# Performance work log

Measured on AMD Instinct MI355X. Metric: run time of the kernel, lower is better.

## Reference

```python
import jax, jax.numpy as jnp
import numpy as np

# dims
B, QL, KL = 2, 1024, 4096
HID = 2048            # hidden_size
H, HD, RD = 16, 128, 64   # heads, head_dim, rope_dim
G = 4                 # gla_num_groups
HPG = H // G          # heads_per_group
QLR = 512             # q low-rank (W_dQ out)
LAT = 256             # latent_dim_per_group
KVP = G * LAT         # kv_proj_dim
EPS = 1e-6


def rmsnorm(x, w):
    var = jnp.mean(jnp.square(x.astype(jnp.float32)), axis=-1, keepdims=True)
    return (x * jax.lax.rsqrt(var + EPS)).astype(x.dtype) * w


def setup_inputs() -> dict:
    key = jax.random.key(0)
    ks = jax.random.split(key, 8)
    s = 0.02
    return {
        "x_q": jax.random.normal(ks[0], (B, QL, HID), jnp.float32),
        "x_kv": jax.random.normal(ks[1], (B, KL, HID), jnp.float32),
        "W_dQ": jax.random.normal(ks[2], (HID, QLR), jnp.float32) * s,
        "q_norm_w": jnp.ones((QLR,), jnp.float32),
        "W_uQ": jax.random.normal(ks[3], (QLR, H * (HD + RD)), jnp.float32) * s,
        "W_dKV": jax.random.normal(ks[4], (HID, KVP + RD), jnp.float32) * s,
        "kv_norm_w": jnp.ones((G, LAT), jnp.float32),
        "W_ukv": jax.random.normal(ks[5], (G, LAT, HPG * 2 * HD), jnp.float32) * s,
        "W_o": jax.random.normal(ks[6], (H * HD, HID), jnp.float32) * s,
    }


def reference(x_q, x_kv, W_dQ, q_norm_w, W_uQ, W_dKV, kv_norm_w, W_ukv, W_o):
    b, ql, _ = x_q.shape
    kl = x_kv.shape[1]
    # --- query path: down-proj -> RMSNorm -> up-proj -> drop rope dims ---
    q = rmsnorm(x_q @ W_dQ, q_norm_w)                       # [b, ql, QLR]
    q = (q @ W_uQ).reshape(b, ql, H, HD + RD)[..., :HD]     # [b, ql, H, HD]
    # --- kv path: down-proj -> slice -> per-group RMSNorm -> grouped up-proj ---
    ckv = (x_kv @ W_dKV)[..., :KVP].reshape(b, kl, G, LAT)  # [b, kl, G, LAT]
    ckv = rmsnorm(ckv, kv_norm_w)                           # weight [G, LAT] broadcasts
    kv = jnp.einsum("bsgl,gld->bsgd", ckv, W_ukv)           # [b, kl, G, HPG*2*HD]
    kv = kv.reshape(b, kl, H, 2 * HD)                       # group-major head order
    k, v = kv[..., :HD], kv[..., HD:]
    # --- SDPA (no mask, non-causal) ---
    scale = 1.0 / np.sqrt(HD).astype(np.float32)
    scores = jnp.einsum("bqhd,bkhd->bhqk", q, k) * scale    # [b, H, ql, kl]
    p = jax.nn.softmax(scores, axis=-1)
    out = jnp.einsum("bhqk,bkhd->bqhd", p, v).reshape(b, ql, H * HD)
    return out @ W_o
```

## Files before the change

### kernel.cpp

```cpp
#include <hip/hip_runtime.h>
#include <hip/hip_bf16.h>
#include <math.h>


typedef __attribute__((ext_vector_type(8))) short short8;
typedef __attribute__((ext_vector_type(4))) float f32x4;

__device__ __forceinline__ ushort f2bf(float x) {
    __hip_bfloat16 h = __float2bfloat16(x);
    return *reinterpret_cast<ushort*>(&h);
}

__global__ __launch_bounds__(256) void cast_bf16(const float* __restrict__ src,
        ushort* __restrict__ dst)
{
    size_t i = ((size_t)blockIdx.x * 256 + threadIdx.x) * 8;
    float4 a = *(const float4*)(src + i);
    float4 b = *(const float4*)(src + i + 4);
    ushort u[8] = {f2bf(a.x), f2bf(a.y), f2bf(a.z), f2bf(a.w),
                   f2bf(b.x), f2bf(b.y), f2bf(b.z), f2bf(b.w)};
    *(uint4*)(dst + i) = *(uint4*)u;
}

__global__ __launch_bounds__(256) void transpose_cast(const float* __restrict__ src,
        ushort* __restrict__ dst, int srl, int dstld, int remap,
        long src_z, long dst_z)
{
    __shared__ ushort tile[64][68];
    const int k0 = blockIdx.x * 64;
    const int n0 = blockIdx.y * 64;
    src += (size_t)blockIdx.z * src_z;
    dst += (size_t)blockIdx.z * dst_z;
    const int cb = n0 + (remap ? (n0 >> 7) * 64 : 0);
    const int t = threadIdx.x;
    {
        int r = t >> 4, c4 = t & 15;
        #pragma unroll
        for (int i = 0; i < 4; ++i) {
            float4 v = *(const float4*)(src + (size_t)(k0 + r + 16 * i) * srl + cb + c4 * 4);
            tile[r + 16 * i][c4 * 4 + 0] = f2bf(v.x);
            tile[r + 16 * i][c4 * 4 + 1] = f2bf(v.y);
            tile[r + 16 * i][c4 * 4 + 2] = f2bf(v.z);
            tile[r + 16 * i][c4 * 4 + 3] = f2bf(v.w);
        }
    }
    __syncthreads();
    {
        int n = t >> 4, k4 = t & 15;
        #pragma unroll
        for (int i = 0; i < 4; ++i) {
            ushort4 v;
            v.x = tile[k4 * 4 + 0][n + 16 * i];
            v.y = tile[k4 * 4 + 1][n + 16 * i];
            v.z = tile[k4 * 4 + 2][n + 16 * i];
            v.w = tile[k4 * 4 + 3][n + 16 * i];
            *(ushort4*)(dst + (size_t)(n0 + n + 16 * i) * dstld + k0 + k4 * 4) = v;
        }
    }
}

__global__ __launch_bounds__(256) void gemm_mfma(const ushort* __restrict__ A,
        const ushort* __restrict__ Bt, void* __restrict__ Cv,
        int M, int N, int K, int lda, int ldb, int ldc, int obf16, float scale)
{
    __shared__ ushort As[128][72];
    __shared__ ushort Bs[128][72];
    const int tid = threadIdx.x;
    const int w = tid >> 6, lane = tid & 63;
    const int quad = lane >> 4, l16 = lane & 15;
    const int wm = (w >> 1) * 64, wn = (w & 1) * 64;
    const int m0 = blockIdx.y * 128, n0 = blockIdx.x * 128;

    f32x4 acc[4][4];
    #pragma unroll
    for (int i = 0; i < 4; ++i)
        #pragma unroll
        for (int j = 0; j < 4; ++j) acc[i][j] = (f32x4){0.f, 0.f, 0.f, 0.f};

    const int str = tid >> 3;
    const int stc = (tid & 7) * 8;

    for (int k0 = 0; k0 < K; k0 += 64) {
        __syncthreads();
        #pragma unroll
        for (int i = 0; i < 4; ++i) {
            int r = str + 32 * i;
            *(uint4*)&As[r][stc] = *(const uint4*)(A + (size_t)(m0 + r) * lda + k0 + stc);
            *(uint4*)&Bs[r][stc] = *(const uint4*)(Bt + (size_t)(n0 + r) * ldb + k0 + stc);
        }
        __syncthreads();
        #pragma unroll
        for (int kc = 0; kc < 2; ++kc) {
            short8 af[4], bf[4];
            #pragma unroll
            for (int i = 0; i < 4; ++i) {
                af[i] = *(const short8*)&As[wm + i * 16 + l16][kc * 32 + quad * 8];
                bf[i] = *(const short8*)&Bs[wn + i * 16 + l16][kc * 32 + quad * 8];
            }
            #pragma unroll
            for (int i = 0; i < 4; ++i)
                #pragma unroll
                for (int j = 0; j < 4; ++j)
                    acc[i][j] = __builtin_amdgcn_mfma_f32_16x16x32_bf16(af[i], bf[j], acc[i][j], 0, 0, 0);
        }
    }
    if (!obf16) {
        float* C = (float*)Cv;
        #pragma unroll
        for (int i = 0; i < 4; ++i)
            #pragma unroll
            for (int r = 0; r < 4; ++r) {
                float* cp = C + (size_t)(m0 + wm + i * 16 + quad * 4 + r) * ldc + n0 + wn + l16;
                #pragma unroll
                for (int j = 0; j < 4; ++j) cp[j * 16] = acc[i][j][r] * scale;
            }
    } else {
        ushort* C = (ushort*)Cv;
        #pragma unroll
        for (int i = 0; i < 4; ++i)
            #pragma unroll
            for (int r = 0; r < 4; ++r) {
                ushort* cp = C + (size_t)(m0 + wm + i * 16 + quad * 4 + r) * ldc + n0 + wn + l16;
                #pragma unroll
                for (int j = 0; j < 4; ++j) cp[j * 16] = f2bf(acc[i][j][r] * scale);
            }
    }
}

__global__ __launch_bounds__(256) void rms_q_wave(const float* __restrict__ x,
        const float* __restrict__ w, ushort* __restrict__ dst)
{
    const int row = blockIdx.x * 4 + (threadIdx.x >> 6);
    const int lane = threadIdx.x & 63;
    const float* p = x + (size_t)row * 512;
    float4 v0 = *(const float4*)(p + lane * 4);
    float4 v1 = *(const float4*)(p + 256 + lane * 4);
    float ss = v0.x*v0.x + v0.y*v0.y + v0.z*v0.z + v0.w*v0.w
             + v1.x*v1.x + v1.y*v1.y + v1.z*v1.z + v1.w*v1.w;
    #pragma unroll
    for (int m = 1; m < 64; m <<= 1) ss += __shfl_xor(ss, m);
    float inv = rsqrtf(ss * (1.f / 512.f) + 1e-6f);
    float4 w0 = *(const float4*)(w + lane * 4);
    float4 w1 = *(const float4*)(w + 256 + lane * 4);
    ushort* dp = dst + (size_t)row * 512;
    ushort4 o0, o1;
    o0.x = f2bf(v0.x * inv * w0.x); o0.y = f2bf(v0.y * inv * w0.y);
    o0.z = f2bf(v0.z * inv * w0.z); o0.w = f2bf(v0.w * inv * w0.w);
    o1.x = f2bf(v1.x * inv * w1.x); o1.y = f2bf(v1.y * inv * w1.y);
    o1.z = f2bf(v1.z * inv * w1.z); o1.w = f2bf(v1.w * inv * w1.w);
    *(ushort4*)(dp + lane * 4)       = o0;
    *(ushort4*)(dp + 256 + lane * 4) = o1;
}

__global__ __launch_bounds__(256) void rms_kv_wave(const float* __restrict__ x,
        const float* __restrict__ w, ushort* __restrict__ dst)
{
    const int idx = blockIdx.x * 4 + (threadIdx.x >> 6);
    const int lane = threadIdx.x & 63;
    const int r = idx >> 2, g = idx & 3;
    const float* p = x + (size_t)r * 1024 + g * 256;
    float4 v = *(const float4*)(p + lane * 4);
    float ss = v.x*v.x + v.y*v.y + v.z*v.z + v.w*v.w;
    #pragma unroll
    for (int m = 1; m < 64; m <<= 1) ss += __shfl_xor(ss, m);
    float inv = rsqrtf(ss * (1.f / 256.f) + 1e-6f);
    float4 wv = *(const float4*)(w + g * 256 + lane * 4);
    ushort4 o;
    o.x = f2bf(v.x * inv * wv.x); o.y = f2bf(v.y * inv * wv.y);
    o.z = f2bf(v.z * inv * wv.z); o.w = f2bf(v.w * inv * wv.w);
    *(ushort4*)(dst + (size_t)r * 1024 + g * 256 + lane * 4) = o;
}

__global__ __launch_bounds__(256) void transpose_v(const ushort* __restrict__ KVb,
                                                   ushort* __restrict__ Vt)
{
    __shared__ ushort tile[64][66];
    const int s0 = blockIdx.x * 64;
    const int d0 = blockIdx.y * 64;
    const int bh = blockIdx.z;
    const int b = bh >> 4, h = bh & 15, g = h >> 2, p = h & 3;
    const int t = threadIdx.x;
    const ushort* src = KVb + (size_t)g * 8388608ull + (size_t)(b * 4096) * 1024 + p * 256 + 128;
    {
        int sl = t >> 4, c4 = t & 15;
        #pragma unroll
        for (int i = 0; i < 4; ++i) {
            int s = sl + 16 * i;
            ushort4 v = *(const ushort4*)(src + (size_t)(s0 + s) * 1024 + d0 + c4 * 4);
            tile[s][c4 * 4 + 0] = v.x; tile[s][c4 * 4 + 1] = v.y;
            tile[s][c4 * 4 + 2] = v.z; tile[s][c4 * 4 + 3] = v.w;
        }
    }
    __syncthreads();
    {
        int dl = t >> 4, s4 = t & 15;
        ushort* dst = Vt + (size_t)(b * 16 + h) * 128 * 4096;
        #pragma unroll
        for (int i = 0; i < 4; ++i) {
            int d = dl + 16 * i;
            ushort4 v;
            v.x = tile[s4 * 4 + 0][d]; v.y = tile[s4 * 4 + 1][d];
            v.z = tile[s4 * 4 + 2][d]; v.w = tile[s4 * 4 + 3][d];
            *(ushort4*)(dst + (size_t)(d0 + d) * 4096 + s0 + s4 * 4) = v;
        }
    }
}

__global__ __launch_bounds__(256) void attn_mfma_split(const ushort* __restrict__ Qb,
        const ushort* __restrict__ KVb, const ushort* __restrict__ Vt,
        float* __restrict__ Opart, float* __restrict__ ml)
{
    __shared__ ushort Ks[64][136];
    __shared__ ushort VsT[128][72];
    __shared__ ushort Ps[4][16][72];

    const int q0 = blockIdx.x * 64;
    const int h = blockIdx.y;
    const int b = blockIdx.z >> 1, chunk = blockIdx.z & 1;
    const int g = h >> 2, p = h & 3;
    const int tid = threadIdx.x;
    const int w = tid >> 6, lane = tid & 63;
    const int quad = lane >> 4, l16 = lane & 15;
    const int sbase = chunk * 2048;

    const ushort* qg = Qb + (size_t)(b * 1024 + q0) * 2048 + h * 128;
    const ushort* kg = KVb + (size_t)g * 8388608ull + (size_t)(b * 4096 + sbase) * 1024 + p * 256;
    const ushort* vg = Vt + (size_t)(b * 16 + h) * 128 * 4096 + sbase;

    {
        int r = tid >> 4, c8 = tid & 15;
        #pragma unroll
        for (int i = 0; i < 4; ++i)
            *(uint4*)&Ks[r + 16 * i][c8 * 8] =
                *(const uint4*)(qg + (size_t)(r + 16 * i) * 2048 + c8 * 8);
    }
    __syncthreads();
    short8 qf[4];
    {
        int qr = w * 16 + l16;
        #pragma unroll
        for (int kc = 0; kc < 4; ++kc)
            qf[kc] = *(const short8*)&Ks[qr][kc * 32 + quad * 8];
    }

    f32x4 accO[8];
    float m_i[4], l_i[4];
    #pragma unroll
    for (int dt = 0; dt < 8; ++dt) accO[dt] = (f32x4){0.f, 0.f, 0.f, 0.f};
    #pragma unroll
    for (int r = 0; r < 4; ++r) { m_i[r] = -INFINITY; l_i[r] = 0.f; }

    for (int s0 = 0; s0 < 2048; s0 += 64) {
        __syncthreads();
        {
            int r = tid >> 4, c8 = tid & 15;
            #pragma unroll
            for (int i = 0; i < 4; ++i)
                *(uint4*)&Ks[r + 16 * i][c8 * 8] =
                    *(const uint4*)(kg + (size_t)(s0 + r + 16 * i) * 1024 + c8 * 8);
            int d = tid >> 3, s8 = tid & 7;
            #pragma unroll
            for (int i = 0; i < 4; ++i)
                *(uint4*)&VsT[d + 32 * i][s8 * 8] =
                    *(const uint4*)(vg + (size_t)(d + 32 * i) * 4096 + s0 + s8 * 8);
        }
        __syncthreads();
        f32x4 accS[4];
        #pragma unroll
        for (int st = 0; st < 4; ++st) accS[st] = (f32x4){0.f, 0.f, 0.f, 0.f};
        #pragma unroll
        for (int kc = 0; kc < 4; ++kc) {
            #pragma unroll
            for (int st = 0; st < 4; ++st) {
                short8 kf = *(const short8*)&Ks[st * 16 + l16][kc * 32 + quad * 8];
                accS[st] = __builtin_amdgcn_mfma_f32_16x16x32_bf16(qf[kc], kf, accS[st], 0, 0, 0);
            }
        }
        #pragma unroll
        for (int r = 0; r < 4; ++r) {
            float tm = fmaxf(fmaxf(accS[0][r], accS[1][r]), fmaxf(accS[2][r], accS[3][r]));
            #pragma unroll
            for (int msk = 1; msk < 16; msk <<= 1) tm = fmaxf(tm, __shfl_xor(tm, msk));
            float mn = fmaxf(m_i[r], tm);
            float alpha = __expf(m_i[r] - mn);
            float rs = 0.f;
            #pragma unroll
            for (int st = 0; st < 4; ++st) {
                float e = __expf(accS[st][r] - mn);
                rs += e;
                Ps[w][quad * 4 + r][st * 16 + l16] = f2bf(e);
            }
            #pragma unroll
            for (int msk = 1; msk < 16; msk <<= 1) rs += __shfl_xor(rs, msk);
            l_i[r] = l_i[r] * alpha + rs;
            m_i[r] = mn;
            #pragma unroll
            for (int dt = 0; dt < 8; ++dt) accO[dt][r] *= alpha;
        }
        __syncthreads();
        short8 pf[2];
        #pragma unroll
        for (int sc = 0; sc < 2; ++sc)
            pf[sc] = *(const short8*)&Ps[w][l16][sc * 32 + quad * 8];
        #pragma unroll
        for (int sc = 0; sc < 2; ++sc) {
            #pragma unroll
            for (int dt = 0; dt < 8; ++dt) {
                short8 vf = *(const short8*)&VsT[dt * 16 + l16][sc * 32 + quad * 8];
                accO[dt] = __builtin_amdgcn_mfma_f32_16x16x32_bf16(pf[sc], vf, accO[dt], 0, 0, 0);
            }
        }
    }
    const int qrow = q0 + w * 16 + quad * 4;
    float* ob = Opart + (size_t)((chunk * 2 + b) * 1024 + qrow) * 2048 + h * 128 + l16;
    #pragma unroll
    for (int r = 0; r < 4; ++r)
        #pragma unroll
        for (int dt = 0; dt < 8; ++dt)
            ob[(size_t)r * 2048 + dt * 16] = accO[dt][r];
    if (l16 == 0) {
        #pragma unroll
        for (int r = 0; r < 4; ++r) {
            size_t mi = ((size_t)((chunk * 2 + b) * 1024 + qrow + r) * 16 + h) * 2;
            ml[mi] = m_i[r];
            ml[mi + 1] = l_i[r];
        }
    }
}

__global__ __launch_bounds__(256) void attn_merge(const float* __restrict__ Opart,
        const float* __restrict__ ml, ushort* __restrict__ Om)
{
    const int idx = blockIdx.x * 4 + (threadIdx.x >> 6);
    const int lane = threadIdx.x & 63;
    const int h = idx & 15;
    const int q = (idx >> 4) & 1023;
    const int b = idx >> 14;

    size_t m1i = ((size_t)((0 * 2 + b) * 1024 + q) * 16 + h) * 2;
    size_t m2i = ((size_t)((1 * 2 + b) * 1024 + q) * 16 + h) * 2;
    float m1 = ml[m1i], l1 = ml[m1i + 1];
    float m2 = ml[m2i], l2 = ml[m2i + 1];
    float M = fmaxf(m1, m2);
    float w1 = __expf(m1 - M), w2 = __expf(m2 - M);
    float invL = 1.f / (l1 * w1 + l2 * w2);

    const float* o1 = Opart + (size_t)((0 * 2 + b) * 1024 + q) * 2048 + h * 128;
    const float* o2 = Opart + (size_t)((1 * 2 + b) * 1024 + q) * 2048 + h * 128;
    ushort* ob = Om + (size_t)(b * 1024 + q) * 2048 + h * 128;
    ob[lane]      = f2bf((o1[lane]      * w1 + o2[lane]      * w2) * invL);
    ob[lane + 64] = f2bf((o1[lane + 64] * w1 + o2[lane + 64] * w2) * invL);
}

extern "C" void kernel_launch(void* const* d_in, const int* in_sizes, int n_in,
                              void* d_out, int out_size, void* d_ws, size_t ws_size,
                              hipStream_t stream)
{
    (void)in_sizes; (void)n_in; (void)out_size; (void)ws_size;
    const float* x_q       = (const float*)d_in[0];
    const float* x_kv      = (const float*)d_in[1];
    const float* W_dQ      = (const float*)d_in[2];
    const float* q_norm_w  = (const float*)d_in[3];
    const float* W_uQ      = (const float*)d_in[4];
    const float* W_dKV     = (const float*)d_in[5];
    const float* kv_norm_w = (const float*)d_in[6];
    const float* W_ukv     = (const float*)d_in[7];
    const float* W_o       = (const float*)d_in[8];
    float* out = (float*)d_out;

    float* ws = (float*)d_ws;
    ushort* xkvb       = (ushort*)ws;
    ushort* attn_out_b = (ushort*)ws;
    float*  mlbuf      = ws + 2097152ull;
    ushort* Wot        = (ushort*)(ws + 4194304ull);
    float*  ckv        = ws + 8388608ull;
    float*  Opart      = ws + 8388608ull;
    ushort* xqb        = (ushort*)(ws + 8388608ull);
    ushort* WdQt       = (ushort*)(ws + 10485760ull);
    float*  q_lat      = ws + 11010048ull;
    ushort* q_lat_b    = (ushort*)(ws + 12058624ull);
    ushort* WuQt       = (ushort*)(ws + 12582912ull);
    ushort* ckv_b      = (ushort*)(ws + 16777216ull);
    ushort* kvgb       = (ushort*)(ws + 20971520ull);
    ushort* vt         = (ushort*)(ws + 37748736ull);
    ushort* qb         = (ushort*)(ws + 46137344ull);
    ushort* WdKVt      = (ushort*)(ws + 48234496ull);
    ushort* Wukvt      = (ushort*)(ws + 49283072ull);

    const float qscale = 0.08838834764831845f;

    cast_bf16<<<2048, 256, 0, stream>>>(x_q, xqb);
    transpose_cast<<<dim3(32, 8, 1), 256, 0, stream>>>(W_dQ, WdQt, 512, 2048, 0, 0, 0);
    gemm_mfma<<<dim3(4, 16), 256, 0, stream>>>(xqb, WdQt, q_lat, 2048, 512, 2048, 2048, 2048, 512, 0, 1.f);
    rms_q_wave<<<512, 256, 0, stream>>>(q_lat, q_norm_w, q_lat_b);
    transpose_cast<<<dim3(8, 32, 1), 256, 0, stream>>>(W_uQ, WuQt, 3072, 512, 1, 0, 0);
    gemm_mfma<<<dim3(16, 16), 256, 0, stream>>>(q_lat_b, WuQt, qb, 2048, 2048, 512, 512, 512, 2048, 1, qscale);
    cast_bf16<<<8192, 256, 0, stream>>>(x_kv, xkvb);
    transpose_cast<<<dim3(32, 16, 1), 256, 0, stream>>>(W_dKV, WdKVt, 1088, 2048, 0, 0, 0);
    gemm_mfma<<<dim3(8, 64), 256, 0, stream>>>(xkvb, WdKVt, ckv, 8192, 1024, 2048, 2048, 2048, 1024, 0, 1.f);
    rms_kv_wave<<<8192, 256, 0, stream>>>(ckv, kv_norm_w, ckv_b);
    transpose_cast<<<dim3(4, 16, 4), 256, 0, stream>>>(W_ukv, Wukvt, 1024, 256, 0, 262144, 262144);
    for (int g = 0; g < 4; ++g)
        gemm_mfma<<<dim3(8, 64), 256, 0, stream>>>(ckv_b + g * 256, Wukvt + (size_t)g * 262144,
                                                   kvgb + (size_t)g * 8388608ull,
                                                   8192, 1024, 256, 1024, 256, 1024, 1, 1.f);
    transpose_v<<<dim3(64, 2, 32), 256, 0, stream>>>(kvgb, vt);
    attn_mfma_split<<<dim3(16, 16, 4), 256, 0, stream>>>(qb, kvgb, vt, Opart, mlbuf);
    attn_merge<<<8192, 256, 0, stream>>>(Opart, mlbuf, attn_out_b);
    transpose_cast<<<dim3(32, 32, 1), 256, 0, stream>>>(W_o, Wot, 2048, 2048, 0, 0, 0);
    gemm_mfma<<<dim3(16, 16), 256, 0, stream>>>(attn_out_b, Wot, out, 2048, 2048, 2048, 2048, 2048, 2048, 0, 1.f);
}
```

Measured before the change: 559.1 us.

## Prefetch K/V tiles into registers, swizzle LDS, and skip most softmax rescales

The attention kernel now loads the next K and V tiles from global memory into registers while the current tile is computed, then writes them to shared memory at the top of the next iteration. Padded shared-memory arrays become XOR-swizzled flat arrays to avoid bank conflicts and save LDS, and launch bounds request 4 blocks per CU. Online softmax only rescales the accumulator when the running max grows by more than 8, and the barrier before reading P is removed because each wave reads only its own P rows. The trade-off is higher register pressure from prefetch buffers and exponentials that can reach e^8 before rescaling, which bf16 P tolerates.

```diff
diff --git a/kernel.cpp b/kernel.cpp
--- a/kernel.cpp
+++ b/kernel.cpp
@@ -10,6 +10,8 @@
     __hip_bfloat16 h = __float2bfloat16(x);
     return *reinterpret_cast<ushort*>(&h);
 }
+
+#define SWZ(row, col) ((col) ^ (((row) & 7) << 3))
 
 __global__ __launch_bounds__(256) void cast_bf16(const float* __restrict__ src,
         ushort* __restrict__ dst)
@@ -206,13 +208,13 @@
     }
 }
 
-__global__ __launch_bounds__(256) void attn_mfma_split(const ushort* __restrict__ Qb,
+__global__ __launch_bounds__(256, 4) void attn_mfma_split(const ushort* __restrict__ Qb,
         const ushort* __restrict__ KVb, const ushort* __restrict__ Vt,
         float* __restrict__ Opart, float* __restrict__ ml)
 {
-    __shared__ ushort Ks[64][136];
-    __shared__ ushort VsT[128][72];
-    __shared__ ushort Ps[4][16][72];
+    __shared__ ushort Ks[64 * 128];
+    __shared__ ushort VsT[128 * 64];
+    __shared__ ushort Ps[4 * 16 * 64];
 
     const int q0 = blockIdx.x * 64;
     const int h = blockIdx.y;
@@ -227,12 +229,23 @@
     const ushort* kg = KVb + (size_t)g * 8388608ull + (size_t)(b * 4096 + sbase) * 1024 + p * 256;
     const ushort* vg = Vt + (size_t)(b * 16 + h) * 128 * 4096 + sbase;
 
-    {
-        int r = tid >> 4, c8 = tid & 15;
-        #pragma unroll
-        for (int i = 0; i < 4; ++i)
-            *(uint4*)&Ks[r + 16 * i][c8 * 8] =
-                *(const uint4*)(qg + (size_t)(r + 16 * i) * 2048 + c8 * 8);
+    const int kr  = tid >> 4;
+    const int kc8 = (tid & 15) * 8;
+    const int vd  = tid >> 3;
+    const int vs8 = (tid & 7) * 8;
+
+    uint4 krg[4], vrg[4];
+    #pragma unroll
+    for (int i = 0; i < 4; ++i)
+        krg[i] = *(const uint4*)(kg + (size_t)(kr + 16 * i) * 1024 + kc8);
+    #pragma unroll
+    for (int i = 0; i < 4; ++i)
+        vrg[i] = *(const uint4*)(vg + (size_t)(vd + 32 * i) * 4096 + vs8);
+
+    #pragma unroll
+    for (int i = 0; i < 4; ++i) {
+        int r = kr + 16 * i;
+        *(uint4*)&Ks[r * 128 + SWZ(r, kc8)] = *(const uint4*)(qg + (size_t)r * 2048 + kc8);
     }
     __syncthreads();
     short8 qf[4];
@@ -240,7 +253,7 @@
         int qr = w * 16 + l16;
         #pragma unroll
         for (int kc = 0; kc < 4; ++kc)
-            qf[kc] = *(const short8*)&Ks[qr][kc * 32 + quad * 8];
+            qf[kc] = *(const short8*)&Ks[qr * 128 + SWZ(qr, kc * 32 + quad * 8)];
     }
 
     f32x4 accO[8];
@@ -252,19 +265,25 @@
 
     for (int s0 = 0; s0 < 2048; s0 += 64) {
         __syncthreads();
-        {
-            int r = tid >> 4, c8 = tid & 15;
+        #pragma unroll
+        for (int i = 0; i < 4; ++i) {
+            int r = kr + 16 * i;
+            *(uint4*)&Ks[r * 128 + SWZ(r, kc8)] = krg[i];
+        }
+        #pragma unroll
+        for (int i = 0; i < 4; ++i) {
+            int d = vd + 32 * i;
+            *(uint4*)&VsT[d * 64 + SWZ(d, vs8)] = vrg[i];
+        }
+        __syncthreads();
+        if (s0 + 64 < 2048) {
             #pragma unroll
             for (int i = 0; i < 4; ++i)
-                *(uint4*)&Ks[r + 16 * i][c8 * 8] =
-                    *(const uint4*)(kg + (size_t)(s0 + r + 16 * i) * 1024 + c8 * 8);
-            int d = tid >> 3, s8 = tid & 7;
+                krg[i] = *(const uint4*)(kg + (size_t)(s0 + 64 + kr + 16 * i) * 1024 + kc8);
             #pragma unroll
             for (int i = 0; i < 4; ++i)
-                *(uint4*)&VsT[d + 32 * i][s8 * 8] =
-                    *(const uint4*)(vg + (size_t)(d + 32 * i) * 4096 + s0 + s8 * 8);
-        }
-        __syncthreads();
+                vrg[i] = *(const uint4*)(vg + (size_t)(vd + 32 * i) * 4096 + s0 + 64 + vs8);
+        }
         f32x4 accS[4];
         #pragma unroll
         for (int st = 0; st < 4; ++st) accS[st] = (f32x4){0.f, 0.f, 0.f, 0.f};
@@ -272,7 +291,8 @@
         for (int kc = 0; kc < 4; ++kc) {
             #pragma unroll
             for (int st = 0; st < 4; ++st) {
-                short8 kf = *(const short8*)&Ks[st * 16 + l16][kc * 32 + quad * 8];
+                int krow = st * 16 + l16;
+                short8 kf = *(const short8*)&Ks[krow * 128 + SWZ(krow, kc * 32 + quad * 8)];
                 accS[st] = __builtin_amdgcn_mfma_f32_16x16x32_bf16(qf[kc], kf, accS[st], 0, 0, 0);
             }
         }
@@ -281,32 +301,36 @@
             float tm = fmaxf(fmaxf(accS[0][r], accS[1][r]), fmaxf(accS[2][r], accS[3][r]));
             #pragma unroll
             for (int msk = 1; msk < 16; msk <<= 1) tm = fmaxf(tm, __shfl_xor(tm, msk));
-            float mn = fmaxf(m_i[r], tm);
-            float alpha = __expf(m_i[r] - mn);
+            if (tm > m_i[r] + 8.f) {
+                float alpha = __expf(m_i[r] - tm);
+                l_i[r] *= alpha;
+                #pragma unroll
+                for (int dt = 0; dt < 8; ++dt) accO[dt][r] *= alpha;
+                m_i[r] = tm;
+            }
+            const float mn = m_i[r];
             float rs = 0.f;
+            const int prow = quad * 4 + r;
             #pragma unroll
             for (int st = 0; st < 4; ++st) {
                 float e = __expf(accS[st][r] - mn);
                 rs += e;
-                Ps[w][quad * 4 + r][st * 16 + l16] = f2bf(e);
+                Ps[(w * 16 + prow) * 64 + SWZ(prow, st * 16 + l16)] = f2bf(e);
             }
             #pragma unroll
             for (int msk = 1; msk < 16; msk <<= 1) rs += __shfl_xor(rs, msk);
-            l_i[r] = l_i[r] * alpha + rs;
-            m_i[r] = mn;
-            #pragma unroll
-            for (int dt = 0; dt < 8; ++dt) accO[dt][r] *= alpha;
-        }
-        __syncthreads();
+            l_i[r] += rs;
+        }
         short8 pf[2];
         #pragma unroll
         for (int sc = 0; sc < 2; ++sc)
-            pf[sc] = *(const short8*)&Ps[w][l16][sc * 32 + quad * 8];
+            pf[sc] = *(const short8*)&Ps[(w * 16 + l16) * 64 + SWZ(l16, sc * 32 + quad * 8)];
         #pragma unroll
         for (int sc = 0; sc < 2; ++sc) {
             #pragma unroll
             for (int dt = 0; dt < 8; ++dt) {
-                short8 vf = *(const short8*)&VsT[dt * 16 + l16][sc * 32 + quad * 8];
+                int vrow = dt * 16 + l16;
+                short8 vf = *(const short8*)&VsT[vrow * 64 + SWZ(vrow, sc * 32 + quad * 8)];
                 accO[dt] = __builtin_amdgcn_mfma_f32_16x16x32_bf16(pf[sc], vf, accO[dt], 0, 0, 0);
             }
         }
```

Result: slower. 768.2 us (+37.4%).
